# Optimization experiments

Measured on AMD Instinct MI355X. Metric: run time of the kernel, lower is better.

## Reference

```python
import jax, jax.numpy as jnp
import numpy as np

B, T, H = 4, 4096, 1024


def setup_inputs() -> dict:
    key = jax.random.key(0)
    k1, k2 = jax.random.split(key)
    h = jax.random.normal(k1, (B, T, H), dtype=jnp.float32)
    # nn.Linear weight, scaled for stable magnitudes
    W = jax.random.normal(k2, (H, H), dtype=jnp.float32) / np.sqrt(H).astype(np.float32)
    return {"h": h, "W": W, "T_hist": 256}


def reference(h, W, T_hist):
    Bb, Tt, Hh = h.shape
    # K = Linear(h) = h @ W.T ; Q = V = h
    K = jnp.einsum('bth,oh->bto', h, W)
    scores = jnp.einsum('bqh,bkh->bqk', h, K) / jnp.sqrt(jnp.asarray(Hh, h.dtype))
    # banded mask: causal (j <= i) AND limited history (j >= i - (T_hist-1))
    i = jnp.arange(Tt)[:, None]
    j = jnp.arange(Tt)[None, :]
    valid = (j <= i) & (j >= i - (T_hist - 1))
    scores = jnp.where(valid[None, :, :], scores, -jnp.inf)
    attn = jax.nn.softmax(scores, axis=-1)
    attn = jnp.nan_to_num(attn, nan=0.0)  # matches torch nan_to_num(0.0)
    context = jnp.einsum('bqk,bkh->bqh', attn, h)
    return context
```

## Files before the change

### kernel.cpp

```cpp
#include <hip/hip_runtime.h>
#include <hip/hip_bf16.h>

#define B_ 4
#define T_ 4096
#define H_ 1024
#define WP2 320

typedef short  s16x8 __attribute__((ext_vector_type(8)));
typedef float  f32x4 __attribute__((ext_vector_type(4)));
typedef unsigned short u16;

static __device__ __forceinline__ u16 bf16rn(float f) {
  unsigned int u = __float_as_uint(f);
  u += 0x7fffu + ((u >> 16) & 1u);
  return (u16)(u >> 16);
}

static __device__ __forceinline__ void gl2lds16(const u16* g, u16* l) {
  __builtin_amdgcn_global_load_lds(
      (__attribute__((address_space(1))) void*)(g),
      (__attribute__((address_space(3))) void*)(l), 16, 0, 0);
}

__global__ __launch_bounds__(256) void k_convT(const float* __restrict__ h,
                                               u16* __restrict__ hb,
                                               u16* __restrict__ hbT) {
  __shared__ u16 tile[64][72];
  const int b  = blockIdx.z;
  const int t0 = blockIdx.y * 64;
  const int c0 = blockIdx.x * 64;
  const int t  = threadIdx.x;
  {
    const int r  = t >> 2;
    const int cq = (t & 3) << 4;
    const size_t g = (size_t)(b * T_ + t0 + r) * H_ + c0 + cq;
    const f32x4* src = (const f32x4*)(h + g);
    u16 o[16];
#pragma unroll
    for (int v = 0; v < 4; ++v) {
      f32x4 x = src[v];
#pragma unroll
      for (int j = 0; j < 4; ++j) o[v * 4 + j] = bf16rn(x[j]);
    }
    s16x8 w0, w1;
#pragma unroll
    for (int j = 0; j < 8; ++j) { w0[j] = (short)o[j]; w1[j] = (short)o[8 + j]; }
    *(s16x8*)(hb + g)     = w0;
    *(s16x8*)(hb + g + 8) = w1;
    *(s16x8*)&tile[r][cq]     = w0;
    *(s16x8*)&tile[r][cq + 8] = w1;
  }
  __syncthreads();
  {
    const int c  = t >> 2;
    const int ch = t & 3;
#pragma unroll
    for (int p = 0; p < 2; ++p) {
      const int k0 = (ch + p * 4) * 8;
      s16x8 w;
#pragma unroll
      for (int j = 0; j < 8; ++j) w[j] = (short)tile[k0 + j][c];
      *(s16x8*)(hbT + (size_t)(b * H_ + c0 + c) * T_ + t0 + k0) = w;
    }
  }
}

__global__ __launch_bounds__(256) void k_convW(const float* __restrict__ src,
                                               u16* __restrict__ dst) {
  const int i = (blockIdx.x * 256 + threadIdx.x) * 8;
  f32x4 a = *(const f32x4*)(src + i);
  f32x4 b = *(const f32x4*)(src + i + 4);
  s16x8 w;
#pragma unroll
  for (int j = 0; j < 4; ++j) {
    w[j]     = (short)bf16rn(a[j]);
    w[4 + j] = (short)bf16rn(b[j]);
  }
  *(s16x8*)(dst + i) = w;
}

__global__ __launch_bounds__(256) void k_gemmK(const u16* __restrict__ hb,
                                               const u16* __restrict__ Wb,
                                               u16* __restrict__ Kb) {
  __shared__ __align__(16) u16 As[512 * 8];
  __shared__ __align__(16) u16 Bs[512 * 8];
  const int t = threadIdx.x;
  const int row0 = blockIdx.y * 128;
  const int col0 = blockIdx.x * 128;
  const int lane = t & 63, wv = t >> 6;
  const int wr = wv >> 1, wc = wv & 1;
  const int l15 = lane & 15, quad = lane >> 4;

  const int c0 = t, c1 = t + 256;
  const size_t gA0 = (size_t)(row0 + (c0 >> 2)) * H_ + (c0 & 3) * 8;
  const size_t gA1 = (size_t)(row0 + (c1 >> 2)) * H_ + (c1 & 3) * 8;
  const size_t gB0 = (size_t)(col0 + (c0 >> 2)) * H_ + (c0 & 3) * 8;
  const size_t gB1 = (size_t)(col0 + (c1 >> 2)) * H_ + (c1 & 3) * 8;

  f32x4 acc[4][4];
#pragma unroll
  for (int m = 0; m < 4; ++m)
#pragma unroll
    for (int n = 0; n < 4; ++n) acc[m][n] = (f32x4)0.0f;

  for (int k0 = 0; k0 < H_; k0 += 32) {
    __syncthreads();
    gl2lds16(hb + gA0 + k0, &As[c0 * 8]);
    gl2lds16(hb + gA1 + k0, &As[c1 * 8]);
    gl2lds16(Wb + gB0 + k0, &Bs[c0 * 8]);
    gl2lds16(Wb + gB1 + k0, &Bs[c1 * 8]);
    __syncthreads();
    s16x8 aF[4], bF[4];
#pragma unroll
    for (int mt = 0; mt < 4; ++mt)
      aF[mt] = *(const s16x8*)&As[((wr * 64 + mt * 16 + l15) * 4 + quad) * 8];
#pragma unroll
    for (int nt = 0; nt < 4; ++nt)
      bF[nt] = *(const s16x8*)&Bs[((wc * 64 + nt * 16 + l15) * 4 + quad) * 8];
#pragma unroll
    for (int mt = 0; mt < 4; ++mt)
#pragma unroll
      for (int nt = 0; nt < 4; ++nt)
        acc[mt][nt] = __builtin_amdgcn_mfma_f32_16x16x32_bf16(aF[mt], bF[nt],
                                                              acc[mt][nt], 0, 0, 0);
  }
#pragma unroll
  for (int mt = 0; mt < 4; ++mt)
#pragma unroll
    for (int nt = 0; nt < 4; ++nt)
#pragma unroll
      for (int r = 0; r < 4; ++r) {
        const int row = row0 + wr * 64 + mt * 16 + quad * 4 + r;
        const int col = col0 + wc * 64 + nt * 16 + l15;
        Kb[(size_t)row * H_ + col] = bf16rn(acc[mt][nt][r]);
      }
}

__global__ __launch_bounds__(512) void k_scores(const u16* __restrict__ hb,
                                                const u16* __restrict__ Kb,
                                                u16* __restrict__ P) {
  __shared__ __align__(16) u16 Ks[2304 * 8];
  __shared__ float Sred[2][4][16];
  const int t = threadIdx.x;
  const int wv = t >> 6, lane = t & 63;
  const int l15 = lane & 15, quad = lane >> 4;
  const int blk = blockIdx.x;
  const int b = blk >> 7;
  const int q0 = (blk & 127) * 32;
  const int qt = wv & 1;
  const int sub = wv >> 1;
  const int qt0 = q0 + qt * 16;
  const int ktbase = (sub == 0) ? 0 : (1 + sub * 4);
  const int nkt = (sub == 0) ? 5 : 4;

  const int npass = (t < 256) ? 5 : 4;
  size_t goff[5];
#pragma unroll
  for (int p = 0; p < 5; ++p) {
    int c = p * 512 + t;
    if (c > 2303) c = 2303;
    const int m = c >> 7, kk = (c >> 6) & 1, lr = (c >> 2) & 15, qd = c & 3;
    int tok = q0 - 256 + m * 16 + lr;
    if (tok < 0) tok = 0;
    goff[p] = (size_t)(b * T_ + tok) * H_ + kk * 32 + qd * 8;
  }
  const u16* qbase = hb + (size_t)(b * T_ + qt0 + l15) * H_ + quad * 8;

  f32x4 acc[5];
#pragma unroll
  for (int i = 0; i < 5; ++i) acc[i] = (f32x4)0.0f;

  for (int hh = 0; hh < H_; hh += 64) {
    __syncthreads();
#pragma unroll
    for (int p = 0; p < 5; ++p)
      if (p < npass) gl2lds16(Kb + goff[p] + hh, &Ks[(p * 512 + t) * 8]);
    __syncthreads();
#pragma unroll
    for (int kk = 0; kk < 2; ++kk) {
      const s16x8 aQ = *(const s16x8*)(qbase + hh + kk * 32);
#pragma unroll
      for (int i = 0; i < 5; ++i) {
        if (i < nkt) {
          const int m = qt + ktbase + i;
          const s16x8 bK =
              *(const s16x8*)&Ks[((m * 2 + kk) * 64 + l15 * 4 + quad) * 8];
          acc[i] = __builtin_amdgcn_mfma_f32_16x16x32_bf16(aQ, bK, acc[i], 0, 0, 0);
        }
      }
    }
  }

  const float scale = 0.03125f;
#pragma unroll
  for (int r = 0; r < 4; ++r) {
    const int q = qt0 + quad * 4 + r;
    float sum = 0.0f;
#pragma unroll
    for (int i = 0; i < 5; ++i) {
      if (i < nkt) {
        const int k = qt0 - 256 + (ktbase + i) * 16 + l15;
        const bool valid = (k >= 0) && (k <= q) && (k >= q - 255);
        const float p = valid ? __expf(acc[i][r] * scale) : 0.0f;
        acc[i][r] = p;
        sum += p;
      }
    }
    sum += __shfl_xor(sum, 1);
    sum += __shfl_xor(sum, 2);
    sum += __shfl_xor(sum, 4);
    sum += __shfl_xor(sum, 8);
    if (l15 == 0) Sred[qt][sub][quad * 4 + r] = sum;
  }
  __syncthreads();
  const int toff = ((q0 & 32) >> 4) + qt;
#pragma unroll
  for (int r = 0; r < 4; ++r) {
    const int q = qt0 + quad * 4 + r;
    const int row = quad * 4 + r;
    const float inv = 1.0f / (Sred[qt][0][row] + Sred[qt][1][row] +
                              Sred[qt][2][row] + Sred[qt][3][row]);
    u16* prow = P + (size_t)(b * T_ + q) * WP2;
#pragma unroll
    for (int i = 0; i < 5; ++i)
      if (i < nkt) prow[(toff + ktbase + i) * 16 + l15] = bf16rn(acc[i][r] * inv);
    if (sub == 0) {
#pragma unroll
      for (int z = 0; z < 3; ++z) {
        const int slot = (toff + 17 + z) % 20;
        prow[slot * 16 + l15] = 0;
      }
    }
  }
}

__global__ __launch_bounds__(512) void k_ctx(const u16* __restrict__ P,
                                             const u16* __restrict__ hbT,
                                             float* __restrict__ out) {
  __shared__ __align__(16) u16 Vs[2560 * 8];
  const int t = threadIdx.x;
  const int wv = t >> 6, lane = t & 63;
  const int l15 = lane & 15, quad = lane >> 4;
  const int fhalf = blockIdx.x;
  const int blk = blockIdx.y;
  const int b = blk >> 6;
  const int q0 = (blk & 63) * 64;
  const int qtile = wv & 3, fh = wv >> 2;
  const int qt0 = q0 + qtile * 16;

  const u16* prow = P + (size_t)(b * T_ + qt0 + l15) * WP2 + quad * 8;
  s16x8 aP[10];
#pragma unroll
  for (int c = 0; c < 10; ++c) aP[c] = *(const s16x8*)(prow + c * 32);

  const int tok0 = q0 - 256;
  size_t goff[5];
#pragma unroll
  for (int p = 0; p < 5; ++p) {
    const int c = p * 512 + t;
    const int cg = c >> 8, ft = (c >> 6) & 3, lr = (c >> 2) & 15, qd = c & 3;
    const int fr = ft * 16 + lr;
    int tok = tok0 + (cg * 4 + qd) * 8;
    if (tok < 0) tok = 0;
    goff[p] = (size_t)(b * H_ + fr) * T_ + tok;
  }

  for (int f8 = 0; f8 < 8; ++f8) {
    const int f0 = (fhalf * 8 + f8) * 64;
    __syncthreads();
#pragma unroll
    for (int p = 0; p < 5; ++p)
      gl2lds16(hbT + goff[p] + (size_t)f0 * T_, &Vs[(p * 512 + t) * 8]);
    __syncthreads();
    f32x4 acc0 = (f32x4)0.0f, acc1 = (f32x4)0.0f;
#pragma unroll
    for (int c = 0; c < 10; ++c) {
      const s16x8 bv0 =
          *(const s16x8*)&Vs[(c * 256 + (fh * 2 + 0) * 64 + l15 * 4 + quad) * 8];
      acc0 = __builtin_amdgcn_mfma_f32_16x16x32_bf16(aP[c], bv0, acc0, 0, 0, 0);
      const s16x8 bv1 =
          *(const s16x8*)&Vs[(c * 256 + (fh * 2 + 1) * 64 + l15 * 4 + quad) * 8];
      acc1 = __builtin_amdgcn_mfma_f32_16x16x32_bf16(aP[c], bv1, acc1, 0, 0, 0);
    }
#pragma unroll
    for (int r = 0; r < 4; ++r) {
      const size_t orow = (size_t)(b * T_ + qt0 + quad * 4 + r) * H_ + f0;
      out[orow + (fh * 2 + 0) * 16 + l15] = acc0[r];
      out[orow + (fh * 2 + 1) * 16 + l15] = acc1[r];
    }
  }
}

extern "C" void kernel_launch(void* const* d_in, const int* in_sizes, int n_in,
                              void* d_out, int out_size, void* d_ws, size_t ws_size,
                              hipStream_t stream) {
  const float* h  = (const float*)d_in[0];
  const float* Wf = (const float*)d_in[1];

  char* ws = (char*)d_ws;
  u16* hb  = (u16*)(ws);
  u16* hbT = (u16*)(ws + (size_t)33554432);
  u16* Kb  = (u16*)(ws + (size_t)67108864);
  u16* Wb  = (u16*)(ws + (size_t)100663296);
  u16* P   = (u16*)(ws + (size_t)102760448);
  float* out = (float*)d_out;

  k_convT <<<dim3(H_ / 64, T_ / 64, B_), 256, 0, stream>>>(h, hb, hbT);
  k_convW <<<dim3(512), 256, 0, stream>>>(Wf, Wb);
  k_gemmK <<<dim3(H_ / 128, (B_ * T_) / 128), 256, 0, stream>>>(hb, Wb, Kb);
  k_scores<<<dim3((B_ * T_) / 32), 512, 0, stream>>>(hb, Kb, P);
  k_ctx   <<<dim3(2, (B_ * T_) / 64), 512, 0, stream>>>(P, hbT, out);
}
```

Baseline: 264.2 us.

## Reorder LDS fragment layout to lane-major and deepen gemm K tile with block swizzle

Across the gemm, scores and PV kernels, the staged LDS tiles now store each fragment in lane order, so a wave's 16-byte fragment reads are contiguous. The intent is to remove LDS bank conflicts from the strided l15*4+quad indexing. The K-projection gemm also loads a 64-wide K slice per barrier pair, halving the number of syncs at the cost of doubled LDS. It also remaps block IDs so blocks sharing W columns run close together, which should improve L2 reuse. The global loads become strided across rows (16 rows by 16 bytes per group), which may reduce coalescing.

```diff
diff --git a/kernel.cpp b/kernel.cpp
--- a/kernel.cpp
+++ b/kernel.cpp
@@ -21,6 +21,7 @@
       (__attribute__((address_space(1))) void*)(g),
       (__attribute__((address_space(3))) void*)(l), 16, 0, 0);
 }
+
 
 __global__ __launch_bounds__(256) void k_convT(const float* __restrict__ h,
                                                u16* __restrict__ hb,
@@ -82,20 +83,25 @@
 __global__ __launch_bounds__(256) void k_gemmK(const u16* __restrict__ hb,
                                                const u16* __restrict__ Wb,
                                                u16* __restrict__ Kb) {
-  __shared__ __align__(16) u16 As[512 * 8];
-  __shared__ __align__(16) u16 Bs[512 * 8];
+  __shared__ __align__(16) u16 As[1024 * 8];
+  __shared__ __align__(16) u16 Bs[1024 * 8];
   const int t = threadIdx.x;
-  const int row0 = blockIdx.y * 128;
-  const int col0 = blockIdx.x * 128;
+  const int id = blockIdx.y * 8 + blockIdx.x;
+  const int slot = id >> 3;
+  const int row0 = ((id & 7) * 16 + (slot >> 3)) * 128;
+  const int col0 = (slot & 7) * 128;
   const int lane = t & 63, wv = t >> 6;
   const int wr = wv >> 1, wc = wv & 1;
   const int l15 = lane & 15, quad = lane >> 4;
 
-  const int c0 = t, c1 = t + 256;
-  const size_t gA0 = (size_t)(row0 + (c0 >> 2)) * H_ + (c0 & 3) * 8;
-  const size_t gA1 = (size_t)(row0 + (c1 >> 2)) * H_ + (c1 & 3) * 8;
-  const size_t gB0 = (size_t)(col0 + (c0 >> 2)) * H_ + (c0 & 3) * 8;
-  const size_t gB1 = (size_t)(col0 + (c1 >> 2)) * H_ + (c1 & 3) * 8;
+  size_t gA[4], gB[4];
+#pragma unroll
+  for (int p = 0; p < 4; ++p) {
+    const int c = p * 256 + t;
+    const int tile = c >> 7, kq = (c >> 4) & 7, lr = c & 15;
+    gA[p] = (size_t)(row0 + tile * 16 + lr) * H_ + kq * 8;
+    gB[p] = (size_t)(col0 + tile * 16 + lr) * H_ + kq * 8;
+  }
 
   f32x4 acc[4][4];
 #pragma unroll
@@ -103,26 +109,31 @@
 #pragma unroll
     for (int n = 0; n < 4; ++n) acc[m][n] = (f32x4)0.0f;
 
-  for (int k0 = 0; k0 < H_; k0 += 32) {
-    __syncthreads();
-    gl2lds16(hb + gA0 + k0, &As[c0 * 8]);
-    gl2lds16(hb + gA1 + k0, &As[c1 * 8]);
-    gl2lds16(Wb + gB0 + k0, &Bs[c0 * 8]);
-    gl2lds16(Wb + gB1 + k0, &Bs[c1 * 8]);
-    __syncthreads();
-    s16x8 aF[4], bF[4];
-#pragma unroll
-    for (int mt = 0; mt < 4; ++mt)
-      aF[mt] = *(const s16x8*)&As[((wr * 64 + mt * 16 + l15) * 4 + quad) * 8];
-#pragma unroll
-    for (int nt = 0; nt < 4; ++nt)
-      bF[nt] = *(const s16x8*)&Bs[((wc * 64 + nt * 16 + l15) * 4 + quad) * 8];
-#pragma unroll
-    for (int mt = 0; mt < 4; ++mt)
+  for (int k0 = 0; k0 < H_; k0 += 64) {
+    __syncthreads();
+#pragma unroll
+    for (int p = 0; p < 4; ++p) {
+      const int c = p * 256 + t;
+      gl2lds16(hb + gA[p] + k0, &As[c * 8]);
+      gl2lds16(Wb + gB[p] + k0, &Bs[c * 8]);
+    }
+    __syncthreads();
+#pragma unroll
+    for (int kk = 0; kk < 2; ++kk) {
+      s16x8 aF[4], bF[4];
+#pragma unroll
+      for (int mt = 0; mt < 4; ++mt)
+        aF[mt] = *(const s16x8*)&As[((wr * 4 + mt) * 128 + kk * 64 + lane) * 8];
 #pragma unroll
       for (int nt = 0; nt < 4; ++nt)
-        acc[mt][nt] = __builtin_amdgcn_mfma_f32_16x16x32_bf16(aF[mt], bF[nt],
-                                                              acc[mt][nt], 0, 0, 0);
+        bF[nt] = *(const s16x8*)&Bs[((wc * 4 + nt) * 128 + kk * 64 + lane) * 8];
+#pragma unroll
+      for (int mt = 0; mt < 4; ++mt)
+#pragma unroll
+        for (int nt = 0; nt < 4; ++nt)
+          acc[mt][nt] = __builtin_amdgcn_mfma_f32_16x16x32_bf16(aF[mt], bF[nt],
+                                                                acc[mt][nt], 0, 0, 0);
+    }
   }
 #pragma unroll
   for (int mt = 0; mt < 4; ++mt)
@@ -159,7 +170,7 @@
   for (int p = 0; p < 5; ++p) {
     int c = p * 512 + t;
     if (c > 2303) c = 2303;
-    const int m = c >> 7, kk = (c >> 6) & 1, lr = (c >> 2) & 15, qd = c & 3;
+    const int m = c >> 7, kk = (c >> 6) & 1, qd = (c >> 4) & 3, lr = c & 15;
     int tok = q0 - 256 + m * 16 + lr;
     if (tok < 0) tok = 0;
     goff[p] = (size_t)(b * T_ + tok) * H_ + kk * 32 + qd * 8;
@@ -183,8 +194,7 @@
       for (int i = 0; i < 5; ++i) {
         if (i < nkt) {
           const int m = qt + ktbase + i;
-          const s16x8 bK =
-              *(const s16x8*)&Ks[((m * 2 + kk) * 64 + l15 * 4 + quad) * 8];
+          const s16x8 bK = *(const s16x8*)&Ks[((m * 2 + kk) * 64 + lane) * 8];
           acc[i] = __builtin_amdgcn_mfma_f32_16x16x32_bf16(aQ, bK, acc[i], 0, 0, 0);
         }
       }
@@ -258,9 +268,9 @@
 #pragma unroll
   for (int p = 0; p < 5; ++p) {
     const int c = p * 512 + t;
-    const int cg = c >> 8, ft = (c >> 6) & 3, lr = (c >> 2) & 15, qd = c & 3;
+    const int cg = c >> 8, ft = (c >> 6) & 3, qd = (c >> 4) & 3, lr = c & 15;
     const int fr = ft * 16 + lr;
-    int tok = tok0 + (cg * 4 + qd) * 8;
+    int tok = tok0 + cg * 32 + qd * 8;
     if (tok < 0) tok = 0;
     goff[p] = (size_t)(b * H_ + fr) * T_ + tok;
   }
@@ -276,10 +286,10 @@
 #pragma unroll
     for (int c = 0; c < 10; ++c) {
       const s16x8 bv0 =
-          *(const s16x8*)&Vs[(c * 256 + (fh * 2 + 0) * 64 + l15 * 4 + quad) * 8];
+          *(const s16x8*)&Vs[(c * 256 + (fh * 2 + 0) * 64 + lane) * 8];
       acc0 = __builtin_amdgcn_mfma_f32_16x16x32_bf16(aP[c], bv0, acc0, 0, 0, 0);
       const s16x8 bv1 =
-          *(const s16x8*)&Vs[(c * 256 + (fh * 2 + 1) * 64 + l15 * 4 + quad) * 8];
+          *(const s16x8*)&Vs[(c * 256 + (fh * 2 + 1) * 64 + lane) * 8];
       acc1 = __builtin_amdgcn_mfma_f32_16x16x32_bf16(aP[c], bv1, acc1, 0, 0, 0);
     }
 #pragma unroll
```

Result: slower. 286.2 us (+8.3%).
